# Optimization experiments

Measured on AMD Instinct MI355X. Metric: run time of the kernel, lower is better.

Reference implementation:

```python
import jax, jax.numpy as jnp
import numpy as np

B, SQ, SKV, D = 8, 2048, 2048, 1024

def setup_inputs() -> dict:
    key = jax.random.key(0)
    ks = jax.random.split(key, 8)
    s = 1.0 / np.sqrt(D)  # torch Linear default init range
    return {
        "target": jax.random.normal(ks[0], (B, SQ, D), dtype=jnp.float32),
        "non_target": jax.random.normal(ks[1], (B, SKV, D), dtype=jnp.float32),
        "Wq": jax.random.uniform(ks[2], (D, D), jnp.float32, -s, s),
        "bq": jax.random.uniform(ks[3], (D,), jnp.float32, -s, s),
        "Wk": jax.random.uniform(ks[4], (D, D), jnp.float32, -s, s),
        "bk": jax.random.uniform(ks[5], (D,), jnp.float32, -s, s),
        "Wv": jax.random.uniform(ks[6], (D, D), jnp.float32, -s, s),
        "bv": jax.random.uniform(ks[7], (D,), jnp.float32, -s, s),
    }

def reference(target, non_target, Wq, bq, Wk, bk, Wv, bv):
    # Linear projections (torch Linear: x @ W.T + b)
    q = jnp.einsum('bsd,ed->bse', target, Wq) + bq       # [B,SQ,D]
    k = jnp.einsum('bsd,ed->bse', non_target, Wk) + bk   # [B,SKV,D]
    v = jnp.einsum('bsd,ed->bse', non_target, Wv) + bv   # [B,SKV,D]
    # Unscaled attention, exactly as the original module (no 1/sqrt(d))
    scores = jnp.einsum('bqd,bkd->bqk', q, k)            # [B,SQ,SKV]
    weights = jax.nn.softmax(scores, axis=-1)
    return jnp.einsum('bqk,bkd->bqd', weights, v)        # [B,SQ,D]
```

## Files before the change

### kernel.cpp

```cpp
#include <hip/hip_runtime.h>


typedef _Float16 half8 __attribute__((ext_vector_type(8)));
typedef _Float16 half4v __attribute__((ext_vector_type(4)));
typedef float floatx4 __attribute__((ext_vector_type(4)));

__device__ __forceinline__ void async_copy16(const _Float16* g, _Float16* l) {
  __builtin_amdgcn_global_load_lds(
      (const __attribute__((address_space(1))) void*)g,
      (__attribute__((address_space(3))) void*)l,
      16, 0, 0);
}

__global__ __launch_bounds__(256) void cast_f32_f16(const float* __restrict__ src,
                                                    _Float16* __restrict__ dst, long n) {
  long i = ((long)blockIdx.x * 256 + threadIdx.x) * 8;
  if (i >= n) return;
  float4 a = *(const float4*)(src + i);
  float4 b = *(const float4*)(src + i + 4);
  half8 h;
  h[0] = (_Float16)a.x; h[1] = (_Float16)a.y; h[2] = (_Float16)a.z; h[3] = (_Float16)a.w;
  h[4] = (_Float16)b.x; h[5] = (_Float16)b.y; h[6] = (_Float16)b.z; h[7] = (_Float16)b.w;
  *(half8*)(dst + i) = h;
}

template <int OMODE>
__global__ __launch_bounds__(512, 2) void gemm256(const _Float16* __restrict__ A,
                                                  const _Float16* __restrict__ Bm,
                                                  const float* __restrict__ bias,
                                                  void* __restrict__ out,
                                                  int K, int N,
                                                  long sA, long sB, long sO) {
  __shared__ __attribute__((aligned(16))) _Float16 lds[65536];
  _Float16* Ar = lds;
  _Float16* Br = lds + 32768;

  const int tid = threadIdx.x;
  const int lane = tid & 63;
  const int wave = tid >> 6;
  const int wm = wave >> 2;
  const int wn = wave & 3;
  const int frow = lane & 15;
  const int fq = (lane >> 4) & 3;
  const long bz = blockIdx.z;

  const _Float16* Ab = A + bz * sA + (long)blockIdx.x * 256 * K;
  const _Float16* Bb = Bm + bz * sB + (long)blockIdx.y * 256 * K;

  const int glog = (tid & 7) ^ ((tid >> 3) & 7);
  const long sg = (long)(2 * (tid >> 3) + (glog >> 2)) * K + (glog & 3) * 8;
  const int ldst = tid * 8;
  const long lK128 = (long)K * 128;

  const int gphys = ((frow & 1) * 4 + fq) ^ (frow >> 1);
  const int aoff = (frow >> 1) * 64 + gphys * 8;

  floatx4 acc[8][4];
#pragma unroll
  for (int m = 0; m < 8; ++m)
#pragma unroll
    for (int n = 0; n < 4; ++n) acc[m][n] = (floatx4){0.f, 0.f, 0.f, 0.f};

  const int NK = K >> 5;

#pragma unroll
  for (int kp = 0; kp < 3; ++kp) {
#pragma unroll
    for (int j = 0; j < 2; ++j)
      async_copy16(Ab + sg + kp * 32 + j * lK128, Ar + kp * 8192 + ldst + j * 4096);
#pragma unroll
    for (int j = 0; j < 2; ++j)
      async_copy16(Bb + sg + kp * 32 + j * lK128, Br + kp * 8192 + ldst + j * 4096);
  }
  asm volatile("s_waitcnt vmcnt(8)" ::: "memory");
  __builtin_amdgcn_s_barrier();

  for (int kc = 0; kc < NK; ++kc) {
    const int slot = kc & 3;
    int ks = kc + 3;
    if (ks > NK - 1) ks = NK - 1;
    const int ssl = ks & 3;
    const _Float16* as = Ar + slot * 8192 + wm * 4096 + aoff;
    const _Float16* bs = Br + slot * 8192 + wn * 2048 + aoff;

    half8 af[4], bf[4];

#pragma unroll
    for (int i = 0; i < 4; ++i) af[i] = *(const half8*)(as + i * 512);
#pragma unroll
    for (int n = 0; n < 4; ++n) bf[n] = *(const half8*)(bs + n * 512);
#pragma unroll
    for (int j = 0; j < 2; ++j)
      async_copy16(Ab + sg + ks * 32 + j * lK128, Ar + ssl * 8192 + ldst + j * 4096);
    __builtin_amdgcn_s_barrier();
    asm volatile("s_waitcnt lgkmcnt(0)" ::: "memory");
    __builtin_amdgcn_sched_barrier(0);
    __builtin_amdgcn_s_setprio(1);
#pragma unroll
    for (int i = 0; i < 4; ++i)
#pragma unroll
      for (int n = 0; n < 4; ++n)
        acc[i][n] = __builtin_amdgcn_mfma_f32_16x16x32_f16(af[i], bf[n], acc[i][n], 0, 0, 0);
    __builtin_amdgcn_s_setprio(0);
    __builtin_amdgcn_s_barrier();

#pragma unroll
    for (int i = 0; i < 4; ++i) af[i] = *(const half8*)(as + 2048 + i * 512);
#pragma unroll
    for (int j = 0; j < 2; ++j)
      async_copy16(Bb + sg + ks * 32 + j * lK128, Br + ssl * 8192 + ldst + j * 4096);
    __builtin_amdgcn_s_barrier();
    asm volatile("s_waitcnt lgkmcnt(0)" ::: "memory");
    __builtin_amdgcn_sched_barrier(0);
    __builtin_amdgcn_s_setprio(1);
#pragma unroll
    for (int i = 0; i < 4; ++i)
#pragma unroll
      for (int n = 0; n < 4; ++n)
        acc[4 + i][n] = __builtin_amdgcn_mfma_f32_16x16x32_f16(af[i], bf[n], acc[4 + i][n], 0, 0, 0);
    __builtin_amdgcn_s_setprio(0);
    asm volatile("s_waitcnt vmcnt(8)" ::: "memory");
    __builtin_amdgcn_s_barrier();
  }

  if (OMODE == 0 || OMODE == 1) {
#pragma unroll
    for (int n = 0; n < 4; ++n) {
      const int cg = blockIdx.y * 256 + wn * 64 + n * 16 + frow;
      const float bvv = bias[cg];
#pragma unroll
      for (int m = 0; m < 8; ++m) {
        const int rg = blockIdx.x * 256 + wm * 128 + m * 16 + fq * 4;
        if (OMODE == 0) {
#pragma unroll
          for (int i = 0; i < 4; ++i)
            ((_Float16*)out)[(long)(rg + i) * N + cg] = (_Float16)(acc[m][n][i] + bvv);
        } else {
          const long bb = rg >> 11;
          const int s = rg & 2047;
          half4v hv;
#pragma unroll
          for (int i = 0; i < 4; ++i) hv[i] = (_Float16)(acc[m][n][i] + bvv);
          *(half4v*)((_Float16*)out + bb * (2048l * 1024) + (long)cg * 2048 + s) = hv;
        }
      }
    }
  } else {
#pragma unroll
    for (int n = 0; n < 4; ++n) {
      const int cg = blockIdx.y * 256 + wn * 64 + n * 16 + frow;
#pragma unroll
      for (int m = 0; m < 8; ++m) {
        const int rgl = blockIdx.x * 256 + wm * 128 + m * 16 + fq * 4;
#pragma unroll
        for (int i = 0; i < 4; ++i) {
          if (OMODE == 2)
            ((float*)out + bz * sO)[(long)(rgl + i) * N + cg] = acc[m][n][i];
          else
            ((_Float16*)out + bz * sO)[(long)(rgl + i) * N + cg] = (_Float16)acc[m][n][i];
        }
      }
    }
  }
}

__global__ __launch_bounds__(256) void softmax_rows(const _Float16* __restrict__ S,
                                                    _Float16* __restrict__ P) {
  const long row = blockIdx.x;
  const _Float16* src = S + row * 2048;
  _Float16* dst = P + row * 2048;
  const int tid = threadIdx.x;

  half8 v = ((const half8*)src)[tid];
  float f[8];
#pragma unroll
  for (int i = 0; i < 8; i++) f[i] = (float)v[i];

  float m = fmaxf(fmaxf(fmaxf(f[0], f[1]), fmaxf(f[2], f[3])),
                  fmaxf(fmaxf(f[4], f[5]), fmaxf(f[6], f[7])));
#pragma unroll
  for (int o = 32; o > 0; o >>= 1) m = fmaxf(m, __shfl_xor(m, o, 64));
  __shared__ float redm[4];
  if ((tid & 63) == 0) redm[tid >> 6] = m;
  __syncthreads();
  m = fmaxf(fmaxf(redm[0], redm[1]), fmaxf(redm[2], redm[3]));

  float e[8], s = 0.f;
#pragma unroll
  for (int i = 0; i < 8; i++) { e[i] = __expf(f[i] - m); s += e[i]; }
#pragma unroll
  for (int o = 32; o > 0; o >>= 1) s += __shfl_xor(s, o, 64);
  __shared__ float reds[4];
  if ((tid & 63) == 0) reds[tid >> 6] = s;
  __syncthreads();
  s = (reds[0] + reds[1]) + (reds[2] + reds[3]);
  const float inv = 1.f / s;

  half8 h;
#pragma unroll
  for (int i = 0; i < 8; i++) h[i] = (_Float16)(e[i] * inv);
  ((half8*)dst)[tid] = h;
}

extern "C" void kernel_launch(void* const* d_in, const int* in_sizes, int n_in,
                              void* d_out, int out_size, void* d_ws, size_t ws_size,
                              hipStream_t stream) {
  const float* target = (const float*)d_in[0];
  const float* non_target = (const float*)d_in[1];
  const float* Wq = (const float*)d_in[2];
  const float* bq = (const float*)d_in[3];
  const float* Wk = (const float*)d_in[4];
  const float* bk = (const float*)d_in[5];
  const float* Wv = (const float*)d_in[6];
  const float* bv = (const float*)d_in[7];

  char* ws = (char*)d_ws;
  const size_t MB = 1ull << 20;
  _Float16* tgt16 = (_Float16*)(ws);
  _Float16* ntg16 = (_Float16*)(ws + 32 * MB);
  _Float16* S16 = (_Float16*)(ws);
  _Float16* P16 = (_Float16*)(ws + 64 * MB);
  _Float16* Q16 = (_Float16*)(ws + 128 * MB);
  _Float16* K16 = (_Float16*)(ws + 160 * MB);
  _Float16* Vt16 = (_Float16*)(ws + 192 * MB);
  _Float16* Wq16 = (_Float16*)(ws + 224 * MB);
  _Float16* Wk16 = (_Float16*)(ws + 226 * MB);
  _Float16* Wv16 = (_Float16*)(ws + 228 * MB);

  const long nBig = 8l * 2048 * 1024;
  const long nW = 1024l * 1024;

  cast_f32_f16<<<8192, 256, 0, stream>>>(target, tgt16, nBig);
  cast_f32_f16<<<8192, 256, 0, stream>>>(non_target, ntg16, nBig);
  cast_f32_f16<<<512, 256, 0, stream>>>(Wq, Wq16, nW);
  cast_f32_f16<<<512, 256, 0, stream>>>(Wk, Wk16, nW);
  cast_f32_f16<<<512, 256, 0, stream>>>(Wv, Wv16, nW);

  gemm256<0><<<dim3(64, 4, 1), 512, 0, stream>>>(tgt16, Wq16, bq, Q16, 1024, 1024, 0, 0, 0);
  gemm256<0><<<dim3(64, 4, 1), 512, 0, stream>>>(ntg16, Wk16, bk, K16, 1024, 1024, 0, 0, 0);
  gemm256<1><<<dim3(64, 4, 1), 512, 0, stream>>>(ntg16, Wv16, bv, Vt16, 1024, 1024, 0, 0, 0);

  gemm256<3><<<dim3(8, 8, 8), 512, 0, stream>>>(Q16, K16, nullptr, S16, 1024, 2048,
                                                2048l * 1024, 2048l * 1024, 2048l * 2048);

  softmax_rows<<<16384, 256, 0, stream>>>(S16, P16);

  gemm256<2><<<dim3(8, 4, 8), 512, 0, stream>>>(P16, Vt16, nullptr, (float*)d_out, 2048, 1024,
                                                2048l * 2048, 1024l * 2048, 2048l * 1024);
}
```

Baseline: 495.3 us.

## Double-buffer LDS fragments in registers and merge GEMM k-step into single barrier phase

Restructures the GEMM main loop so the A/B fragments for the next k-slice are read from LDS into a second register set while MFMAs run on the current set, with the loop unrolled by two to ping-pong the buffers. Each k-step now issues all four global->LDS async copies at once and uses one barrier instead of the previous two-phase, three-barrier schedule, waiting with vmcnt(4). Base pointers are pre-offset to cut address arithmetic. This raises VGPR pressure (two full fragment sets, 24 half8 registers) and assumes NK is even, and the tighter vmcnt/barrier plan carries some risk of LDS slot reuse hazards.

```diff
diff --git a/kernel.cpp b/kernel.cpp
--- a/kernel.cpp
+++ b/kernel.cpp
@@ -24,6 +24,38 @@
   *(half8*)(dst + i) = h;
 }
 
+
+#define GSLICE(KC, AFC, BFC, AFN, BFN)                                          \
+  {                                                                             \
+    const int kc_ = (KC);                                                       \
+    int ks_ = kc_ + 3; if (ks_ > NK - 1) ks_ = NK - 1;                          \
+    int pf_ = kc_ + 1; if (pf_ > NK - 1) pf_ = NK - 1;                          \
+    _Float16* sa_ = Ar + (ks_ & 3) * 8192 + ldst;                               \
+    _Float16* sb_ = Br + (ks_ & 3) * 8192 + ldst;                               \
+    const long go_ = (long)ks_ * 32;                                            \
+    async_copy16(Abg + go_, sa_);                                               \
+    async_copy16(Abg + go_ + lK128, sa_ + 4096);                                \
+    async_copy16(Bbg + go_, sb_);                                               \
+    async_copy16(Bbg + go_ + lK128, sb_ + 4096);                                \
+    const _Float16* pa_ = Ar + (pf_ & 3) * 8192 + wm * 4096 + aoff;             \
+    const _Float16* pb_ = Br + (pf_ & 3) * 8192 + wn * 2048 + aoff;             \
+    _Pragma("unroll") for (int n = 0; n < 4; ++n)                               \
+      BFN[n] = *(const half8*)(pb_ + n * 512);                                  \
+    _Pragma("unroll") for (int i = 0; i < 8; ++i)                               \
+      AFN[i] = *(const half8*)(pa_ + (i & 3) * 512 + (i >> 2) * 2048);          \
+    __builtin_amdgcn_sched_barrier(0);                                          \
+    __builtin_amdgcn_s_setprio(1);                                              \
+    _Pragma("unroll") for (int i = 0; i < 8; ++i)                               \
+      _Pragma("unroll") for (int n = 0; n < 4; ++n)                             \
+        acc[i][n] = __builtin_amdgcn_mfma_f32_16x16x32_f16(AFC[i], BFC[n],      \
+                                                           acc[i][n], 0, 0, 0); \
+    __builtin_amdgcn_s_setprio(0);                                              \
+    asm volatile("s_waitcnt lgkmcnt(0)" ::: "memory");                          \
+    __builtin_amdgcn_sched_barrier(0);                                          \
+    asm volatile("s_waitcnt vmcnt(4)" ::: "memory");                            \
+    __builtin_amdgcn_s_barrier();                                               \
+  }
+
 template <int OMODE>
 __global__ __launch_bounds__(512, 2) void gemm256(const _Float16* __restrict__ A,
                                                   const _Float16* __restrict__ Bm,
@@ -44,14 +76,14 @@
   const int fq = (lane >> 4) & 3;
   const long bz = blockIdx.z;
 
-  const _Float16* Ab = A + bz * sA + (long)blockIdx.x * 256 * K;
-  const _Float16* Bb = Bm + bz * sB + (long)blockIdx.y * 256 * K;
-
   const int glog = (tid & 7) ^ ((tid >> 3) & 7);
   const long sg = (long)(2 * (tid >> 3) + (glog >> 2)) * K + (glog & 3) * 8;
   const int ldst = tid * 8;
   const long lK128 = (long)K * 128;
 
+  const _Float16* Abg = A + bz * sA + (long)blockIdx.x * 256 * K + sg;
+  const _Float16* Bbg = Bm + bz * sB + (long)blockIdx.y * 256 * K + sg;
+
   const int gphys = ((frow & 1) * 4 + fq) ^ (frow >> 1);
   const int aoff = (frow >> 1) * 64 + gphys * 8;
 
@@ -65,62 +97,29 @@
 
 #pragma unroll
   for (int kp = 0; kp < 3; ++kp) {
-#pragma unroll
-    for (int j = 0; j < 2; ++j)
-      async_copy16(Ab + sg + kp * 32 + j * lK128, Ar + kp * 8192 + ldst + j * 4096);
-#pragma unroll
-    for (int j = 0; j < 2; ++j)
-      async_copy16(Bb + sg + kp * 32 + j * lK128, Br + kp * 8192 + ldst + j * 4096);
-  }
-  asm volatile("s_waitcnt vmcnt(8)" ::: "memory");
+    async_copy16(Abg + kp * 32, Ar + kp * 8192 + ldst);
+    async_copy16(Abg + kp * 32 + lK128, Ar + kp * 8192 + ldst + 4096);
+    async_copy16(Bbg + kp * 32, Br + kp * 8192 + ldst);
+    async_copy16(Bbg + kp * 32 + lK128, Br + kp * 8192 + ldst + 4096);
+  }
+  asm volatile("s_waitcnt vmcnt(4)" ::: "memory");
   __builtin_amdgcn_s_barrier();
 
-  for (int kc = 0; kc < NK; ++kc) {
-    const int slot = kc & 3;
-    int ks = kc + 3;
-    if (ks > NK - 1) ks = NK - 1;
-    const int ssl = ks & 3;
-    const _Float16* as = Ar + slot * 8192 + wm * 4096 + aoff;
-    const _Float16* bs = Br + slot * 8192 + wn * 2048 + aoff;
-
-    half8 af[4], bf[4];
-
-#pragma unroll
-    for (int i = 0; i < 4; ++i) af[i] = *(const half8*)(as + i * 512);
-#pragma unroll
-    for (int n = 0; n < 4; ++n) bf[n] = *(const half8*)(bs + n * 512);
-#pragma unroll
-    for (int j = 0; j < 2; ++j)
-      async_copy16(Ab + sg + ks * 32 + j * lK128, Ar + ssl * 8192 + ldst + j * 4096);
-    __builtin_amdgcn_s_barrier();
-    asm volatile("s_waitcnt lgkmcnt(0)" ::: "memory");
-    __builtin_amdgcn_sched_barrier(0);
-    __builtin_amdgcn_s_setprio(1);
-#pragma unroll
-    for (int i = 0; i < 4; ++i)
-#pragma unroll
-      for (int n = 0; n < 4; ++n)
-        acc[i][n] = __builtin_amdgcn_mfma_f32_16x16x32_f16(af[i], bf[n], acc[i][n], 0, 0, 0);
-    __builtin_amdgcn_s_setprio(0);
-    __builtin_amdgcn_s_barrier();
-
-#pragma unroll
-    for (int i = 0; i < 4; ++i) af[i] = *(const half8*)(as + 2048 + i * 512);
-#pragma unroll
-    for (int j = 0; j < 2; ++j)
-      async_copy16(Bb + sg + ks * 32 + j * lK128, Br + ssl * 8192 + ldst + j * 4096);
-    __builtin_amdgcn_s_barrier();
-    asm volatile("s_waitcnt lgkmcnt(0)" ::: "memory");
-    __builtin_amdgcn_sched_barrier(0);
-    __builtin_amdgcn_s_setprio(1);
-#pragma unroll
-    for (int i = 0; i < 4; ++i)
-#pragma unroll
-      for (int n = 0; n < 4; ++n)
-        acc[4 + i][n] = __builtin_amdgcn_mfma_f32_16x16x32_f16(af[i], bf[n], acc[4 + i][n], 0, 0, 0);
-    __builtin_amdgcn_s_setprio(0);
-    asm volatile("s_waitcnt vmcnt(8)" ::: "memory");
-    __builtin_amdgcn_s_barrier();
+  half8 afA[8], bfA[4], afB[8], bfB[4];
+  {
+    const _Float16* pa = Ar + wm * 4096 + aoff;
+    const _Float16* pb = Br + wn * 2048 + aoff;
+#pragma unroll
+    for (int n = 0; n < 4; ++n) bfA[n] = *(const half8*)(pb + n * 512);
+#pragma unroll
+    for (int i = 0; i < 8; ++i) afA[i] = *(const half8*)(pa + (i & 3) * 512 + (i >> 2) * 2048);
+  }
+  asm volatile("s_waitcnt lgkmcnt(0)" ::: "memory");
+  __builtin_amdgcn_sched_barrier(0);
+
+  for (int kc = 0; kc < NK; kc += 2) {
+    GSLICE(kc, afA, bfA, afB, bfB);
+    GSLICE(kc + 1, afB, bfB, afA, bfA);
   }
 
   if (OMODE == 0 || OMODE == 1) {
```

After: 488.3 us. Within noise of the previous version (-1.4%).
